# Performance work log

Hardware: AMD Instinct MI355X
Metric: run time of the kernel (lower is better)

The kernel has to match this reference:

```python
import jax, jax.numpy as jnp
import numpy as np

B, N, F, H1, H2, NC = 1024, 64, 1024, 256, 128, 128
ALPHA = 0.2   # LeakyReLU slope
BN_EPS = 1e-5


def setup_inputs() -> dict:
    key = jax.random.key(0)
    ks = jax.random.split(key, 20)
    d = {}
    d["x"] = jax.random.normal(ks[0], (B, 1, F), dtype=jnp.float32)
    d["neighbor"] = jax.random.normal(ks[1], (B, N, 1, F), dtype=jnp.float32)
    # GraphAttn layer 1 params
    d["W1"] = jax.random.normal(ks[2], (H1, F), dtype=jnp.float32) / np.sqrt(F)
    d["b1"] = jnp.zeros((H1,), dtype=jnp.float32)
    d["a11"] = jax.random.normal(ks[3], (H1,), dtype=jnp.float32) / np.sqrt(H1)
    d["a12"] = jax.random.normal(ks[4], (H1,), dtype=jnp.float32) / np.sqrt(H1)
    d["g1"] = jnp.ones((), dtype=jnp.float32)   # BatchNorm1d(1) weight (scalar)
    d["be1"] = jnp.zeros((), dtype=jnp.float32)  # BatchNorm1d(1) bias
    # GraphAttn layer 2 params
    d["W2"] = jax.random.normal(ks[5], (H2, H1), dtype=jnp.float32) / np.sqrt(H1)
    d["b2"] = jnp.zeros((H2,), dtype=jnp.float32)
    d["a21"] = jax.random.normal(ks[6], (H2,), dtype=jnp.float32) / np.sqrt(H2)
    d["a22"] = jax.random.normal(ks[7], (H2,), dtype=jnp.float32) / np.sqrt(H2)
    d["g2"] = jnp.ones((), dtype=jnp.float32)
    d["be2"] = jnp.zeros((), dtype=jnp.float32)
    # final classifier
    d["Wl"] = jax.random.normal(ks[8], (NC, H2), dtype=jnp.float32) / np.sqrt(H2)
    d["bl"] = jnp.zeros((NC,), dtype=jnp.float32)
    return d


def _l2norm_c(t):
    # torch nf.normalize default: p=2, dim=1 -> here the singleton channel axis (-2)
    n = jnp.sqrt(jnp.sum(t * t, axis=-2, keepdims=True))
    return t / jnp.maximum(n, 1e-12)


def _gat_layer(x, nb, W, b, a_self, a_nb):
    # x: [B,1,Fin], nb: [B,N,1,Fin]
    xh = jnp.einsum('bcf,hf->bch', x, W) + b        # [B,1,H]
    nbh = jnp.einsum('bncf,hf->bnch', nb, W) + b    # [B,N,1,H]
    # att1(x[i]) + att2(neighbor[i]) -> scores over N (C==1 squeezed)
    s = (jnp.einsum('bch,h->bc', xh, a_self)[:, None, :]
         + jnp.einsum('bnch,h->bnc', nbh, a_nb))[..., 0]   # [B,N]
    A = jax.nn.softmax(jax.nn.leaky_relu(s, ALPHA), axis=1)  # softmax over neighbors
    out = jnp.einsum('bn,bnch->bch', A, nbh)        # [B,1,H]
    return out, nbh


def _bn_relu(t, g, b, axes):
    # BatchNorm1d(1) in training mode: stats over all non-channel dims of the tensor
    m = jnp.mean(t, axis=axes, keepdims=True)
    v = jnp.mean(jnp.square(t - m), axis=axes, keepdims=True)
    return jax.nn.relu(g * (t - m) * jax.lax.rsqrt(v + BN_EPS) + b)


def reference(x, neighbor, W1, b1, a11, a12, g1, be1,
              W2, b2, a21, a22, g2, be2, Wl, bl):
    x = _l2norm_c(x)
    nb = _l2norm_c(neighbor)
    x, nb = _gat_layer(x, nb, W1, b1, a11, a12)
    # acvt1 applied to x [B,1,H1] (stats over B,H) and to each neighbor tensor
    # [N,1,H1] separately (per-sample stats -> axes (1,3) of [B,N,1,H1])
    x = _bn_relu(x, g1, be1, axes=(0, 2))
    nb = _bn_relu(nb, g1, be1, axes=(1, 3))
    x, nb = _gat_layer(x, nb, W2, b2, a21, a22)
    x = _bn_relu(x, g2, be2, axes=(0, 2))
    # Flatten -> Dropout(p=0) -> Linear
    logits = jnp.einsum('bh,ch->bc', x.reshape(x.shape[0], -1), Wl) + bl
    return logits
```

## Files before the change

kernel.cpp:

```cpp
#include <hip/hip_runtime.h>
#include <hip/hip_bf16.h>
#include <stdint.h>

#define B_    1024
#define N_    64
#define F_    1024
#define H1_   256
#define H2_   128
#define NC_   128
#define ALPHA 0.2f
#define BN_EPS 1e-5f

typedef __attribute__((ext_vector_type(4))) float  f32x4;
typedef __attribute__((ext_vector_type(8))) __bf16 bf16x8;
typedef __attribute__((ext_vector_type(4))) __bf16 bf16x4;

__device__ inline float sign_ref(float v) {
    float s = copysignf(1.0f, v);
    return (fabsf(v) >= 1e-12f) ? s : v * 1e12f;
}

__device__ __forceinline__ void gload_lds16(const void* g, void* l) {
    auto gp = reinterpret_cast<const __attribute__((address_space(1))) void*>(
        reinterpret_cast<uintptr_t>(g));
    auto lp = reinterpret_cast<__attribute__((address_space(3))) void*>(
        reinterpret_cast<uintptr_t>(l));
    __builtin_amdgcn_global_load_lds(gp, lp, 16, 0, 0);
}

__device__ inline float blk_reduce(float v, float* buf) {
    #pragma unroll
    for (int o = 32; o > 0; o >>= 1) v += __shfl_xor(v, o, 64);
    __syncthreads();
    const int wave = threadIdx.x >> 6, lane = threadIdx.x & 63;
    if (lane == 0) buf[wave] = v;
    __syncthreads();
    float r = 0.f;
    if (threadIdx.x == 0) {
        const int nw = blockDim.x >> 6;
        for (int i = 0; i < nw; ++i) r += buf[i];
    }
    return r;
}

__global__ __launch_bounds__(256) void k_prep(
    const float* __restrict__ W1, const float* __restrict__ W2,
    const float* __restrict__ b1, const float* __restrict__ a11,
    const float* __restrict__ a12, const float* __restrict__ b2,
    const float* __restrict__ a21, const float* __restrict__ a22,
    __bf16* __restrict__ W1b, __bf16* __restrict__ W2b,
    float* __restrict__ w1a, float* __restrict__ w1a12,
    float* __restrict__ w2a, float* __restrict__ w2a22,
    float* __restrict__ cscal)
{
    __shared__ float rbuf[8];
    const int blk = blockIdx.x, tid = threadIdx.x;
    if (blk < 256) {
        const int i0 = blk * 1024 + tid * 4;
        float4 v = *(const float4*)(W1 + i0);
        bf16x4 p = { (__bf16)v.x, (__bf16)v.y, (__bf16)v.z, (__bf16)v.w };
        *(bf16x4*)(W1b + i0) = p;
    } else if (blk < 288) {
        const int i0 = (blk - 256) * 1024 + tid * 4;
        float4 v = *(const float4*)(W2 + i0);
        bf16x4 p = { (__bf16)v.x, (__bf16)v.y, (__bf16)v.z, (__bf16)v.w };
        *(bf16x4*)(W2b + i0) = p;
    } else if (blk < 292) {
        const int f = (blk - 288) * 256 + tid;
        float s1 = 0.f, s2 = 0.f;
        for (int h = 0; h < H1_; ++h) {
            const float w = W1[h * F_ + f];
            s1 += w * a11[h]; s2 += w * a12[h];
        }
        w1a[f] = s1; w1a12[f] = s2;
    } else if (blk == 292) {
        float s1 = 0.f, s2 = 0.f;
        for (int h = 0; h < H2_; ++h) {
            const float w = W2[h * H1_ + tid];
            s1 += w * a21[h]; s2 += w * a22[h];
        }
        w2a[tid] = s1; w2a22[tid] = s2;
    } else {
        float v1 = b1[tid] * a11[tid];
        float v2 = (tid < H2_) ? b2[tid] * a21[tid] : 0.f;
        float v3 = (tid < H2_) ? b2[tid] * a22[tid] : 0.f;
        float r1 = blk_reduce(v1, rbuf);
        float r2 = blk_reduce(v2, rbuf);
        float r3 = blk_reduce(v3, rbuf);
        if (tid == 0) { cscal[0] = r1; cscal[1] = r2; cscal[2] = r3; }
    }
}

__global__ __launch_bounds__(256) void k_sself1(
    const float* __restrict__ x, const float* __restrict__ w1a,
    const float* __restrict__ cscal, float* __restrict__ sself1)
{
    __shared__ float rbuf[8];
    const int b = blockIdx.x, tid = threadIdx.x;
    const float* xb = x + (size_t)b * F_;
    float p = 0.f;
    for (int i = tid; i < F_; i += 256) p += sign_ref(xb[i]) * w1a[i];
    float r = blk_reduce(p, rbuf);
    if (tid == 0) sself1[b] = r + cscal[0];
}

__global__ __launch_bounds__(256, 1) void k_gemm1(
    const float* __restrict__ A, const __bf16* __restrict__ Bw,
    const float* __restrict__ bias, __bf16* __restrict__ C)
{
    constexpr int BM = 128, BN = 256, BK = 64, K = F_;
    constexpr int LDA = BK + 8;
    __shared__ __attribute__((aligned(16))) char smem[BM * LDA * 2 + BN * BK * 2];
    __bf16* As = (__bf16*)smem;
    __bf16* Bs = (__bf16*)(smem + BM * LDA * 2);
    __bf16* Cs = Bs;

    const int tid = threadIdx.x;
    const int wave = tid >> 6, lane = tid & 63;
    const int wm = wave & 1, wn = wave >> 1;
    const int rowin = lane & 15, kq = lane >> 4;
    const size_t m0 = (size_t)blockIdx.x * BM;

    f32x4 acc[4][8] = {};

    const int cqA = tid & 15, r0A = tid >> 4;
    const float* Abase = A + m0 * K + cqA * 4;

    for (int k0 = 0; k0 < K; k0 += BK) {
        #pragma unroll
        for (int it = 0; it < 8; ++it) {
            const int s = it * 256 + tid;
            const int r = s >> 3;
            const int c8 = (s & 7) ^ (r & 7);
            gload_lds16(Bw + (size_t)r * K + k0 + c8 * 8, Bs + s * 8);
        }
        #pragma unroll
        for (int rr = 0; rr < 8; ++rr) {
            const int r = r0A + rr * 16;
            float4 v = *(const float4*)(Abase + (size_t)r * K + k0);
            bf16x4 p = { (__bf16)sign_ref(v.x), (__bf16)sign_ref(v.y),
                         (__bf16)sign_ref(v.z), (__bf16)sign_ref(v.w) };
            *(bf16x4*)&As[r * LDA + cqA * 4] = p;
        }
        __syncthreads();
        #pragma unroll
        for (int ks = 0; ks < 2; ++ks) {
            bf16x8 af[4], bv[8];
            #pragma unroll
            for (int mi = 0; mi < 4; ++mi)
                af[mi] = *(const bf16x8*)&As[(wm * 64 + mi * 16 + rowin) * LDA + ks * 32 + kq * 8];
            #pragma unroll
            for (int ni = 0; ni < 8; ++ni) {
                const int r = wn * 128 + ni * 16 + rowin;
                const int c = (ks * 4 + kq) ^ (r & 7);
                bv[ni] = *(const bf16x8*)&Bs[(r * 8 + c) * 8];
            }
            #pragma unroll
            for (int mi = 0; mi < 4; ++mi)
                #pragma unroll
                for (int ni = 0; ni < 8; ++ni)
                    acc[mi][ni] = __builtin_amdgcn_mfma_f32_16x16x32_bf16(
                        af[mi], bv[ni], acc[mi][ni], 0, 0, 0);
        }
        __syncthreads();
    }
    const int cr0 = (lane >> 4) * 4, cc = lane & 15;
    for (int half = 0; half < 2; ++half) {
        if (wm == half) {
            #pragma unroll
            for (int ni = 0; ni < 8; ++ni) {
                const int col = wn * 128 + ni * 16 + cc;
                const float bs = bias[col];
                #pragma unroll
                for (int mi = 0; mi < 4; ++mi)
                    #pragma unroll
                    for (int i = 0; i < 4; ++i)
                        Cs[(mi * 16 + cr0 + i) * 256 + col] =
                            (__bf16)(acc[mi][ni][i] + bs);
            }
        }
        __syncthreads();
        #pragma unroll
        for (int it = 0; it < 8; ++it) {
            const int s = it * 256 + tid;
            const size_t row = m0 + half * 64 + (s >> 5);
            *(bf16x8*)(C + row * 256 + (s & 31) * 8) = *(const bf16x8*)&Cs[s * 8];
        }
        __syncthreads();
    }
}

__global__ __launch_bounds__(256) void k_agg1(
    const __bf16* __restrict__ nbh1, const float* __restrict__ sself1,
    const float* __restrict__ a12, const float* __restrict__ g1p,
    const float* __restrict__ be1p, float* __restrict__ out1,
    float* __restrict__ alpha1, float* __restrict__ beta1)
{
    __shared__ __attribute__((aligned(16))) __bf16 tile[N_ * H1_];
    __shared__ float a12s[H1_];
    __shared__ float sv[N_];
    __shared__ float rbuf[8];
    const int b = blockIdx.x, tid = threadIdx.x;
    const __bf16* src = nbh1 + (size_t)b * N_ * H1_;
    #pragma unroll
    for (int it = 0; it < 8; ++it)
        ((bf16x8*)tile)[it * 256 + tid] = ((const bf16x8*)src)[it * 256 + tid];
    a12s[tid] = a12[tid];
    __syncthreads();
    {
        const int n = tid >> 2, q = tid & 3;
        float p = 0.f;
        for (int i = 0; i < 64; ++i) {
            const int h = q * 64 + ((i + tid) & 63);
            p += (float)tile[n * H1_ + h] * a12s[h];
        }
        p += __shfl_xor(p, 1); p += __shfl_xor(p, 2);
        if (q == 0) { float s = sself1[b] + p; sv[n] = s > 0.f ? s : ALPHA * s; }
    }
    __syncthreads();
    if (tid < 64) {
        float s = sv[tid], m = s;
        #pragma unroll
        for (int o = 1; o < 64; o <<= 1) m = fmaxf(m, __shfl_xor(m, o));
        float e = __expf(s - m), t = e;
        #pragma unroll
        for (int o = 1; o < 64; o <<= 1) t += __shfl_xor(t, o);
        sv[tid] = e / t;
    }
    __syncthreads();
    float acc = 0.f, ss = 0.f, sq = 0.f;
    for (int n2 = 0; n2 < N_; ++n2) {
        const float v = (float)tile[n2 * H1_ + tid];
        acc += sv[n2] * v; ss += v; sq += v * v;
    }
    out1[(size_t)b * H1_ + tid] = acc;
    const float rs = blk_reduce(ss, rbuf);
    const float rq = blk_reduce(sq, rbuf);
    if (tid == 0) {
        const float inv = 1.f / (float)(N_ * H1_);
        const float mean = rs * inv, var = rq * inv - mean * mean;
        const float a = (*g1p) * rsqrtf(var + BN_EPS);
        alpha1[b] = a; beta1[b] = (*be1p) - a * mean;
    }
}

__global__ __launch_bounds__(256) void k_bnred(
    const float* __restrict__ src, const int n,
    float* __restrict__ psum, float* __restrict__ psq)
{
    __shared__ float rbuf[8];
    float s = 0.f, q = 0.f;
    for (int i = blockIdx.x * 256 + threadIdx.x; i < n; i += 64 * 256) {
        const float v = src[i]; s += v; q += v * v;
    }
    const float rs = blk_reduce(s, rbuf);
    const float rq = blk_reduce(q, rbuf);
    if (threadIdx.x == 0) { psum[blockIdx.x] = rs; psq[blockIdx.x] = rq; }
}

__global__ __launch_bounds__(256) void k_sself2(
    const float* __restrict__ out1, const float* __restrict__ psum,
    const float* __restrict__ psq, const float* __restrict__ gp,
    const float* __restrict__ bep, const float* __restrict__ w2a,
    const float* __restrict__ cscal, float* __restrict__ sself2)
{
    __shared__ float rbuf[8];
    __shared__ float axbx[2];
    const int b = blockIdx.x, tid = threadIdx.x;
    if (tid < 64) {
        float s = psum[tid], q = psq[tid];
        #pragma unroll
        for (int o = 32; o > 0; o >>= 1) { s += __shfl_xor(s, o); q += __shfl_xor(q, o); }
        if (tid == 0) {
            const float n = (float)(B_ * H1_);
            const float mean = s / n, var = q / n - mean * mean;
            const float a = (*gp) * rsqrtf(var + BN_EPS);
            axbx[0] = a; axbx[1] = (*bep) - a * mean;
        }
    }
    __syncthreads();
    const float ax = axbx[0], bx = axbx[1];
    const float v = out1[(size_t)b * H1_ + tid];
    const float x2 = fmaxf(fmaf(ax, v, bx), 0.f);
    float r = blk_reduce(x2 * w2a[tid], rbuf);
    if (tid == 0) sself2[b] = r + cscal[1];
}

__global__ __launch_bounds__(256) void k_agg2(
    const __bf16* __restrict__ nbh1, const float* __restrict__ alpha1,
    const float* __restrict__ beta1, const float* __restrict__ sself2,
    const float* __restrict__ w2a22, const float* __restrict__ cscal,
    const __bf16* __restrict__ W2b, const float* __restrict__ b2,
    float* __restrict__ out2)
{
    __shared__ __attribute__((aligned(16))) __bf16 tile[N_ * H1_];
    __shared__ float wv[H1_];
    __shared__ float sv[N_];
    __shared__ float g2s[H1_ + 8];
    __shared__ float hpart[H2_];
    const int b = blockIdx.x, tid = threadIdx.x;
    const __bf16* src = nbh1 + (size_t)b * N_ * H1_;
    #pragma unroll
    for (int it = 0; it < 8; ++it)
        ((bf16x8*)tile)[it * 256 + tid] = ((const bf16x8*)src)[it * 256 + tid];
    wv[tid] = w2a22[tid];
    const float al = alpha1[b], be = beta1[b];
    __syncthreads();
    {
        const int n = tid >> 2, q = tid & 3;
        float p = 0.f;
        for (int i = 0; i < 64; ++i) {
            const int h = q * 64 + ((i + tid) & 63);
            const float v = (float)tile[n * H1_ + h];
            p += fmaxf(fmaf(al, v, be), 0.f) * wv[h];
        }
        p += __shfl_xor(p, 1); p += __shfl_xor(p, 2);
        if (q == 0) {
            float s = sself2[b] + p + cscal[2];
            sv[n] = s > 0.f ? s : ALPHA * s;
        }
    }
    __syncthreads();
    if (tid < 64) {
        float s = sv[tid], m = s;
        #pragma unroll
        for (int o = 1; o < 64; o <<= 1) m = fmaxf(m, __shfl_xor(m, o));
        float e = __expf(s - m), t = e;
        #pragma unroll
        for (int o = 1; o < 64; o <<= 1) t += __shfl_xor(t, o);
        sv[tid] = e / t;
    }
    __syncthreads();
    {
        float g = 0.f;
        for (int n2 = 0; n2 < N_; ++n2) {
            const float v = (float)tile[n2 * H1_ + tid];
            g += sv[n2] * fmaxf(fmaf(al, v, be), 0.f);
        }
        g2s[tid + (tid >> 5)] = g;
    }
    __syncthreads();
    #pragma unroll 4
    for (int j = 0; j < 16; ++j) {
        const int idx = j * 256 + tid;
        const int h = idx >> 5, k8 = idx & 31;
        const bf16x8 w = ((const bf16x8*)W2b)[idx];
        float p = 0.f;
        #pragma unroll
        for (int i = 0; i < 8; ++i) {
            const int k = k8 * 8 + i;
            p += (float)w[i] * g2s[k + (k >> 5)];
        }
        p += __shfl_xor(p, 1); p += __shfl_xor(p, 2); p += __shfl_xor(p, 4);
        p += __shfl_xor(p, 8); p += __shfl_xor(p, 16);
        if ((tid & 31) == 0) hpart[h] = p;
    }
    __syncthreads();
    if (tid < H2_) out2[(size_t)b * H2_ + tid] = hpart[tid] + b2[tid];
}

__global__ __launch_bounds__(128) void k_final(
    const float* __restrict__ out2, const float* __restrict__ psum,
    const float* __restrict__ psq, const float* __restrict__ gp,
    const float* __restrict__ bep, const float* __restrict__ Wl,
    const float* __restrict__ bl, float* __restrict__ logits)
{
    __shared__ float xr[H2_];
    __shared__ float Ws[NC_][H2_ + 1];
    __shared__ float axbx[2];
    const int b = blockIdx.x, tid = threadIdx.x;
    if (tid < 64) {
        float s = psum[tid], q = psq[tid];
        #pragma unroll
        for (int o = 32; o > 0; o >>= 1) { s += __shfl_xor(s, o); q += __shfl_xor(q, o); }
        if (tid == 0) {
            const float n = (float)(B_ * H2_);
            const float mean = s / n, var = q / n - mean * mean;
            const float a = (*gp) * rsqrtf(var + BN_EPS);
            axbx[0] = a; axbx[1] = (*bep) - a * mean;
        }
    }
    for (int i = tid; i < NC_ * H2_ / 4; i += 128) {
        float4 v = ((const float4*)Wl)[i];
        const int r = i >> 5, c = (i & 31) * 4;
        Ws[r][c] = v.x; Ws[r][c + 1] = v.y; Ws[r][c + 2] = v.z; Ws[r][c + 3] = v.w;
    }
    __syncthreads();
    xr[tid] = fmaxf(fmaf(axbx[0], out2[(size_t)b * H2_ + tid], axbx[1]), 0.f);
    __syncthreads();
    float acc = bl[tid];
    #pragma unroll 4
    for (int h = 0; h < H2_; ++h) acc += xr[h] * Ws[tid][h];
    logits[(size_t)b * NC_ + tid] = acc;
}

extern "C" void kernel_launch(void* const* d_in, const int* in_sizes, int n_in,
                              void* d_out, int out_size, void* d_ws, size_t ws_size,
                              hipStream_t stream)
{
    const float* x   = (const float*)d_in[0];
    const float* nb  = (const float*)d_in[1];
    const float* W1  = (const float*)d_in[2];
    const float* b1  = (const float*)d_in[3];
    const float* a11 = (const float*)d_in[4];
    const float* a12 = (const float*)d_in[5];
    const float* g1  = (const float*)d_in[6];
    const float* be1 = (const float*)d_in[7];
    const float* W2  = (const float*)d_in[8];
    const float* b2  = (const float*)d_in[9];
    const float* a21 = (const float*)d_in[10];
    const float* a22 = (const float*)d_in[11];
    const float* g2  = (const float*)d_in[12];
    const float* be2 = (const float*)d_in[13];
    const float* Wl  = (const float*)d_in[14];
    const float* bl  = (const float*)d_in[15];
    float* logits = (float*)d_out;

    size_t off = 0;
    auto alc = [&](size_t bytes) {
        void* p = (char*)d_ws + off;
        off = (off + bytes + 255) & ~(size_t)255;
        return p;
    };
    __bf16* W1b   = (__bf16*)alc((size_t)H1_ * F_ * 2);
    __bf16* W2b   = (__bf16*)alc((size_t)H2_ * H1_ * 2);
    float* w1a    = (float*)alc(F_ * 4);
    float* w1a12  = (float*)alc(F_ * 4);
    float* w2a    = (float*)alc(H1_ * 4);
    float* w2a22  = (float*)alc(H1_ * 4);
    float* cscal  = (float*)alc(3 * 4);
    float* sself1 = (float*)alc(B_ * 4);
    float* sself2 = (float*)alc(B_ * 4);
    float* alpha1 = (float*)alc(B_ * 4);
    float* beta1  = (float*)alc(B_ * 4);
    float* psum1  = (float*)alc(64 * 4);
    float* psq1   = (float*)alc(64 * 4);
    float* psum2  = (float*)alc(64 * 4);
    float* psq2   = (float*)alc(64 * 4);
    float* out1   = (float*)alc((size_t)B_ * H1_ * 4);
    float* out2   = (float*)alc((size_t)B_ * H2_ * 4);
    __bf16* nbh1  = (__bf16*)alc((size_t)B_ * N_ * H1_ * 2);

    k_prep<<<294, 256, 0, stream>>>(W1, W2, b1, a11, a12, b2, a21, a22,
                                    W1b, W2b, w1a, w1a12, w2a, w2a22, cscal);
    k_sself1<<<B_, 256, 0, stream>>>(x, w1a, cscal, sself1);
    k_gemm1<<<(B_ * N_) / 128, 256, 0, stream>>>(nb, W1b, b1, nbh1);
    k_agg1<<<B_, 256, 0, stream>>>(nbh1, sself1, a12, g1, be1, out1, alpha1, beta1);
    k_bnred<<<64, 256, 0, stream>>>(out1, B_ * H1_, psum1, psq1);
    k_sself2<<<B_, 256, 0, stream>>>(out1, psum1, psq1, g1, be1, w2a, cscal, sself2);
    k_agg2<<<B_, 256, 0, stream>>>(nbh1, alpha1, beta1, sself2, w2a22, cscal,
                                   W2b, b2, out2);
    k_bnred<<<64, 256, 0, stream>>>(out2, B_ * H2_, psum2, psq2);
    k_final<<<B_, 128, 0, stream>>>(out2, psum2, psq2, g2, be2, Wl, bl, logits);
}
```

Baseline: 503.2 us.

## Fuse self-score and BN partial reductions into aggregation kernels, drop separate launches

Folds the self-attention score computation into the first aggregation kernel and the per-sample BN sum/sum-of-squares into the aggregation kernels. Each consumer then reduces the 1024 per-block partials itself, so the separate bnred and sself2 kernels disappear. Tile loads now use direct global-to-LDS copies, and an unused weight-vector precompute is removed. This cuts the launch count from 9 to 5 and removes extra passes over out1/out2, at the cost of every block redundantly reducing 1024 partials.

```diff
diff --git a/kernel.cpp b/kernel.cpp
--- a/kernel.cpp
+++ b/kernel.cpp
@@ -49,9 +49,8 @@
     const float* __restrict__ a12, const float* __restrict__ b2,
     const float* __restrict__ a21, const float* __restrict__ a22,
     __bf16* __restrict__ W1b, __bf16* __restrict__ W2b,
-    float* __restrict__ w1a, float* __restrict__ w1a12,
-    float* __restrict__ w2a, float* __restrict__ w2a22,
-    float* __restrict__ cscal)
+    float* __restrict__ w1a, float* __restrict__ w2a,
+    float* __restrict__ w2a22, float* __restrict__ cscal)
 {
     __shared__ float rbuf[8];
     const int blk = blockIdx.x, tid = threadIdx.x;
@@ -67,12 +66,9 @@
         *(bf16x4*)(W2b + i0) = p;
     } else if (blk < 292) {
         const int f = (blk - 288) * 256 + tid;
-        float s1 = 0.f, s2 = 0.f;
-        for (int h = 0; h < H1_; ++h) {
-            const float w = W1[h * F_ + f];
-            s1 += w * a11[h]; s2 += w * a12[h];
-        }
-        w1a[f] = s1; w1a12[f] = s2;
+        float s1 = 0.f;
+        for (int h = 0; h < H1_; ++h) s1 += W1[h * F_ + f] * a11[h];
+        w1a[f] = s1;
     } else if (blk == 292) {
         float s1 = 0.f, s2 = 0.f;
         for (int h = 0; h < H2_; ++h) {
@@ -89,19 +85,6 @@
         float r3 = blk_reduce(v3, rbuf);
         if (tid == 0) { cscal[0] = r1; cscal[1] = r2; cscal[2] = r3; }
     }
-}
-
-__global__ __launch_bounds__(256) void k_sself1(
-    const float* __restrict__ x, const float* __restrict__ w1a,
-    const float* __restrict__ cscal, float* __restrict__ sself1)
-{
-    __shared__ float rbuf[8];
-    const int b = blockIdx.x, tid = threadIdx.x;
-    const float* xb = x + (size_t)b * F_;
-    float p = 0.f;
-    for (int i = tid; i < F_; i += 256) p += sign_ref(xb[i]) * w1a[i];
-    float r = blk_reduce(p, rbuf);
-    if (tid == 0) sself1[b] = r + cscal[0];
 }
 
 __global__ __launch_bounds__(256, 1) void k_gemm1(
@@ -190,23 +173,39 @@
     }
 }
 
-__global__ __launch_bounds__(256) void k_agg1(
-    const __bf16* __restrict__ nbh1, const float* __restrict__ sself1,
-    const float* __restrict__ a12, const float* __restrict__ g1p,
-    const float* __restrict__ be1p, float* __restrict__ out1,
-    float* __restrict__ alpha1, float* __restrict__ beta1)
+__global__ __launch_bounds__(256) void k_front(
+    const float* __restrict__ x, const float* __restrict__ w1a,
+    const __bf16* __restrict__ nbh1, const float* __restrict__ a12,
+    const float* __restrict__ g1p, const float* __restrict__ be1p,
+    const float* __restrict__ cscal,
+    float* __restrict__ out1, float* __restrict__ alpha1,
+    float* __restrict__ beta1, float* __restrict__ psum1,
+    float* __restrict__ psq1)
 {
     __shared__ __attribute__((aligned(16))) __bf16 tile[N_ * H1_];
     __shared__ float a12s[H1_];
     __shared__ float sv[N_];
     __shared__ float rbuf[8];
+    __shared__ float sscal[1];
+
     const int b = blockIdx.x, tid = threadIdx.x;
+
+    const float* xb = x + (size_t)b * F_;
+    float xv[4], wa[4];
+    #pragma unroll
+    for (int i = 0; i < 4; ++i) { xv[i] = xb[tid + i * 256]; wa[i] = w1a[tid + i * 256]; }
     const __bf16* src = nbh1 + (size_t)b * N_ * H1_;
     #pragma unroll
     for (int it = 0; it < 8; ++it)
-        ((bf16x8*)tile)[it * 256 + tid] = ((const bf16x8*)src)[it * 256 + tid];
+        gload_lds16(src + (it * 256 + tid) * 8, tile + (it * 256 + tid) * 8);
     a12s[tid] = a12[tid];
-    __syncthreads();
+    float p0 = 0.f;
+    #pragma unroll
+    for (int i = 0; i < 4; ++i) p0 += sign_ref(xv[i]) * wa[i];
+    float r0 = blk_reduce(p0, rbuf);
+    if (tid == 0) sscal[0] = r0 + cscal[0];
+    __syncthreads();
+
     {
         const int n = tid >> 2, q = tid & 3;
         float p = 0.f;
@@ -215,7 +214,7 @@
             p += (float)tile[n * H1_ + h] * a12s[h];
         }
         p += __shfl_xor(p, 1); p += __shfl_xor(p, 2);
-        if (q == 0) { float s = sself1[b] + p; sv[n] = s > 0.f ? s : ALPHA * s; }
+        if (q == 0) { float s = sscal[0] + p; sv[n] = s > 0.f ? s : ALPHA * s; }
     }
     __syncthreads();
     if (tid < 64) {
@@ -228,84 +227,79 @@
         sv[tid] = e / t;
     }
     __syncthreads();
-    float acc = 0.f, ss = 0.f, sq = 0.f;
+
+    float o1 = 0.f, ss = 0.f, sq = 0.f;
     for (int n2 = 0; n2 < N_; ++n2) {
         const float v = (float)tile[n2 * H1_ + tid];
-        acc += sv[n2] * v; ss += v; sq += v * v;
-    }
-    out1[(size_t)b * H1_ + tid] = acc;
-    const float rs = blk_reduce(ss, rbuf);
-    const float rq = blk_reduce(sq, rbuf);
-    if (tid == 0) {
-        const float inv = 1.f / (float)(N_ * H1_);
-        const float mean = rs * inv, var = rq * inv - mean * mean;
-        const float a = (*g1p) * rsqrtf(var + BN_EPS);
-        alpha1[b] = a; beta1[b] = (*be1p) - a * mean;
-    }
-}
-
-__global__ __launch_bounds__(256) void k_bnred(
-    const float* __restrict__ src, const int n,
-    float* __restrict__ psum, float* __restrict__ psq)
-{
-    __shared__ float rbuf[8];
-    float s = 0.f, q = 0.f;
-    for (int i = blockIdx.x * 256 + threadIdx.x; i < n; i += 64 * 256) {
-        const float v = src[i]; s += v; q += v * v;
-    }
-    const float rs = blk_reduce(s, rbuf);
-    const float rq = blk_reduce(q, rbuf);
-    if (threadIdx.x == 0) { psum[blockIdx.x] = rs; psq[blockIdx.x] = rq; }
-}
-
-__global__ __launch_bounds__(256) void k_sself2(
-    const float* __restrict__ out1, const float* __restrict__ psum,
-    const float* __restrict__ psq, const float* __restrict__ gp,
-    const float* __restrict__ bep, const float* __restrict__ w2a,
-    const float* __restrict__ cscal, float* __restrict__ sself2)
-{
-    __shared__ float rbuf[8];
-    __shared__ float axbx[2];
-    const int b = blockIdx.x, tid = threadIdx.x;
-    if (tid < 64) {
-        float s = psum[tid], q = psq[tid];
-        #pragma unroll
-        for (int o = 32; o > 0; o >>= 1) { s += __shfl_xor(s, o); q += __shfl_xor(q, o); }
+        o1 += sv[n2] * v; ss += v; sq += v * v;
+    }
+    out1[(size_t)b * H1_ + tid] = o1;
+    {
+        const float rs = blk_reduce(ss, rbuf);
+        const float rq = blk_reduce(sq, rbuf);
         if (tid == 0) {
-            const float n = (float)(B_ * H1_);
-            const float mean = s / n, var = q / n - mean * mean;
-            const float a = (*gp) * rsqrtf(var + BN_EPS);
-            axbx[0] = a; axbx[1] = (*bep) - a * mean;
-        }
-    }
-    __syncthreads();
-    const float ax = axbx[0], bx = axbx[1];
-    const float v = out1[(size_t)b * H1_ + tid];
-    const float x2 = fmaxf(fmaf(ax, v, bx), 0.f);
-    float r = blk_reduce(x2 * w2a[tid], rbuf);
-    if (tid == 0) sself2[b] = r + cscal[1];
-}
-
-__global__ __launch_bounds__(256) void k_agg2(
-    const __bf16* __restrict__ nbh1, const float* __restrict__ alpha1,
-    const float* __restrict__ beta1, const float* __restrict__ sself2,
-    const float* __restrict__ w2a22, const float* __restrict__ cscal,
-    const __bf16* __restrict__ W2b, const float* __restrict__ b2,
-    float* __restrict__ out2)
+            const float inv = 1.f / (float)(N_ * H1_);
+            const float mean = rs * inv, var = rq * inv - mean * mean;
+            const float a = (*g1p) * rsqrtf(var + BN_EPS);
+            alpha1[b] = a; beta1[b] = (*be1p) - a * mean;
+        }
+        const float rsx = blk_reduce(o1, rbuf);
+        const float rqx = blk_reduce(o1 * o1, rbuf);
+        if (tid == 0) { psum1[b] = rsx; psq1[b] = rqx; }
+    }
+}
+
+__global__ __launch_bounds__(256) void k_back(
+    const __bf16* __restrict__ nbh1, const float* __restrict__ out1,
+    const float* __restrict__ alpha1, const float* __restrict__ beta1,
+    const float* __restrict__ psum1, const float* __restrict__ psq1,
+    const float* __restrict__ g1p, const float* __restrict__ be1p,
+    const float* __restrict__ w2a, const float* __restrict__ w2a22,
+    const float* __restrict__ cscal, const __bf16* __restrict__ W2b,
+    const float* __restrict__ b2,
+    float* __restrict__ out2, float* __restrict__ psum2,
+    float* __restrict__ psq2)
 {
     __shared__ __attribute__((aligned(16))) __bf16 tile[N_ * H1_];
     __shared__ float wv[H1_];
+    __shared__ float w2as[H1_];
     __shared__ float sv[N_];
     __shared__ float g2s[H1_ + 8];
     __shared__ float hpart[H2_];
+    __shared__ float rbuf[8];
+    __shared__ float scal[3];
+
     const int b = blockIdx.x, tid = threadIdx.x;
+
     const __bf16* src = nbh1 + (size_t)b * N_ * H1_;
     #pragma unroll
     for (int it = 0; it < 8; ++it)
-        ((bf16x8*)tile)[it * 256 + tid] = ((const bf16x8*)src)[it * 256 + tid];
-    wv[tid] = w2a22[tid];
+        gload_lds16(src + (it * 256 + tid) * 8, tile + (it * 256 + tid) * 8);
+    wv[tid] = w2a22[tid]; w2as[tid] = w2a[tid];
+    const float o1 = out1[(size_t)b * H1_ + tid];
     const float al = alpha1[b], be = beta1[b];
-    __syncthreads();
+
+    {
+        float s = 0.f, q = 0.f;
+        for (int i = tid; i < B_; i += 256) { s += psum1[i]; q += psq1[i]; }
+        const float gs = blk_reduce(s, rbuf);
+        const float gq = blk_reduce(q, rbuf);
+        if (tid == 0) {
+            const float n = (float)(B_ * H1_);
+            const float mean = gs / n, var = gq / n - mean * mean;
+            const float a = (*g1p) * rsqrtf(var + BN_EPS);
+            scal[0] = a; scal[1] = (*be1p) - a * mean;
+        }
+    }
+    __syncthreads();
+
+    {
+        const float x2 = fmaxf(fmaf(scal[0], o1, scal[1]), 0.f);
+        const float r = blk_reduce(x2 * w2as[tid], rbuf);
+        if (tid == 0) scal[2] = r + cscal[1];
+    }
+    __syncthreads();
+
     {
         const int n = tid >> 2, q = tid & 3;
         float p = 0.f;
@@ -316,7 +310,7 @@
         }
         p += __shfl_xor(p, 1); p += __shfl_xor(p, 2);
         if (q == 0) {
-            float s = sself2[b] + p + cscal[2];
+            float s = scal[2] + p + cscal[2];
             sv[n] = s > 0.f ? s : ALPHA * s;
         }
     }
@@ -331,6 +325,7 @@
         sv[tid] = e / t;
     }
     __syncthreads();
+
     {
         float g = 0.f;
         for (int n2 = 0; n2 < N_; ++n2) {
@@ -340,6 +335,7 @@
         g2s[tid + (tid >> 5)] = g;
     }
     __syncthreads();
+
     #pragma unroll 4
     for (int j = 0; j < 16; ++j) {
         const int idx = j * 256 + tid;
@@ -356,28 +352,37 @@
         if ((tid & 31) == 0) hpart[h] = p;
     }
     __syncthreads();
-    if (tid < H2_) out2[(size_t)b * H2_ + tid] = hpart[tid] + b2[tid];
-}
-
-__global__ __launch_bounds__(128) void k_final(
-    const float* __restrict__ out2, const float* __restrict__ psum,
-    const float* __restrict__ psq, const float* __restrict__ gp,
-    const float* __restrict__ bep, const float* __restrict__ Wl,
+    {
+        float o2 = 0.f;
+        if (tid < H2_) o2 = hpart[tid] + b2[tid];
+        const float rs2 = blk_reduce(o2, rbuf);
+        const float rq2 = blk_reduce(o2 * o2, rbuf);
+        if (tid < H2_) out2[(size_t)b * H2_ + tid] = o2;
+        if (tid == 0) { psum2[b] = rs2; psq2[b] = rq2; }
+    }
+}
+
+__global__ __launch_bounds__(128) void k_fin(
+    const float* __restrict__ out2, const float* __restrict__ psum2,
+    const float* __restrict__ psq2, const float* __restrict__ g2p,
+    const float* __restrict__ be2p, const float* __restrict__ Wl,
     const float* __restrict__ bl, float* __restrict__ logits)
 {
     __shared__ float xr[H2_];
     __shared__ float Ws[NC_][H2_ + 1];
     __shared__ float axbx[2];
+    __shared__ float rbuf[8];
     const int b = blockIdx.x, tid = threadIdx.x;
-    if (tid < 64) {
-        float s = psum[tid], q = psq[tid];
-        #pragma unroll
-        for (int o = 32; o > 0; o >>= 1) { s += __shfl_xor(s, o); q += __shfl_xor(q, o); }
+    {
+        float s = 0.f, q = 0.f;
+        for (int i = tid; i < B_; i += 128) { s += psum2[i]; q += psq2[i]; }
+        const float gs = blk_reduce(s, rbuf);
+        const float gq = blk_reduce(q, rbuf);
         if (tid == 0) {
             const float n = (float)(B_ * H2_);
-            const float mean = s / n, var = q / n - mean * mean;
-            const float a = (*gp) * rsqrtf(var + BN_EPS);
-            axbx[0] = a; axbx[1] = (*bep) - a * mean;
+            const float mean = gs / n, var = gq / n - mean * mean;
+            const float a = (*g2p) * rsqrtf(var + BN_EPS);
+            axbx[0] = a; axbx[1] = (*be2p) - a * mean;
         }
     }
     for (int i = tid; i < NC_ * H2_ / 4; i += 128) {
@@ -425,31 +430,28 @@
     __bf16* W1b   = (__bf16*)alc((size_t)H1_ * F_ * 2);
     __bf16* W2b   = (__bf16*)alc((size_t)H2_ * H1_ * 2);
     float* w1a    = (float*)alc(F_ * 4);
-    float* w1a12  = (float*)alc(F_ * 4);
     float* w2a    = (float*)alc(H1_ * 4);
     float* w2a22  = (float*)alc(H1_ * 4);
     float* cscal  = (float*)alc(3 * 4);
     float* sself1 = (float*)alc(B_ * 4);
-    float* sself2 = (float*)alc(B_ * 4);
     float* alpha1 = (float*)alc(B_ * 4);
     float* beta1  = (float*)alc(B_ * 4);
-    float* psum1  = (float*)alc(64 * 4);
-    float* psq1   = (float*)alc(64 * 4);
-    float* psum2  = (float*)alc(64 * 4);
-    float* psq2   = (float*)alc(64 * 4);
+    float* psum1  = (float*)alc(B_ * 4);
+    float* psq1   = (float*)alc(B_ * 4);
+    float* psum2  = (float*)alc(B_ * 4);
+    float* psq2   = (float*)alc(B_ * 4);
     float* out1   = (float*)alc((size_t)B_ * H1_ * 4);
     float* out2   = (float*)alc((size_t)B_ * H2_ * 4);
     __bf16* nbh1  = (__bf16*)alc((size_t)B_ * N_ * H1_ * 2);
+    (void)sself1;
 
     k_prep<<<294, 256, 0, stream>>>(W1, W2, b1, a11, a12, b2, a21, a22,
-                                    W1b, W2b, w1a, w1a12, w2a, w2a22, cscal);
-    k_sself1<<<B_, 256, 0, stream>>>(x, w1a, cscal, sself1);
+                                    W1b, W2b, w1a, w2a, w2a22, cscal);
     k_gemm1<<<(B_ * N_) / 128, 256, 0, stream>>>(nb, W1b, b1, nbh1);
-    k_agg1<<<B_, 256, 0, stream>>>(nbh1, sself1, a12, g1, be1, out1, alpha1, beta1);
-    k_bnred<<<64, 256, 0, stream>>>(out1, B_ * H1_, psum1, psq1);
-    k_sself2<<<B_, 256, 0, stream>>>(out1, psum1, psq1, g1, be1, w2a, cscal, sself2);
-    k_agg2<<<B_, 256, 0, stream>>>(nbh1, alpha1, beta1, sself2, w2a22, cscal,
-                                   W2b, b2, out2);
-    k_bnred<<<64, 256, 0, stream>>>(out2, B_ * H2_, psum2, psq2);
-    k_final<<<B_, 128, 0, stream>>>(out2, psum2, psq2, g2, be2, Wl, bl, logits);
-}
+    k_front<<<B_, 256, 0, stream>>>(x, w1a, nbh1, a12, g1, be1, cscal,
+                                    out1, alpha1, beta1, psum1, psq1);
+    k_back<<<B_, 256, 0, stream>>>(nbh1, out1, alpha1, beta1, psum1, psq1,
+                                   g1, be1, w2a, w2a22, cscal, W2b, b2,
+                                   out2, psum2, psq2);
+    k_fin<<<B_, 128, 0, stream>>>(out2, psum2, psq2, g2, be2, Wl, bl, logits);
+}
```

After: 491.0 us. 2.4% less time.
